# Kernel tuning notes

Hardware: AMD Instinct MI355X
Metric: run time of the kernel (lower is better)

Reference implementation:

```python
import jax, jax.numpy as jnp
from jax import lax
import numpy as np

B, V, S, K = 16, 8, 256, 66  # batch, predicates/example, seq len, num BIO tags


def setup_inputs() -> dict:
    key = jax.random.key(0)
    ks = jax.random.split(key, 9)
    return {
        "log_pa": jax.random.normal(ks[0], (B, S, S, K), jnp.float32),
        "score": jax.random.normal(ks[1], (B, S, S, K), jnp.float32),
        "v_label": jax.random.randint(ks[2], (B, V), 0, S, jnp.int32),
        "v_l": jnp.full((B,), V, jnp.int32),
        "orig_l": jax.random.randint(ks[3], (B,), S // 2, S + 1, jnp.int32),
        "role_label": jax.random.randint(ks[4], (B, V, S), 0, K, jnp.int32),
        "start_transitions": jax.random.normal(ks[5], (K,), jnp.float32),
        "transitions": jax.random.normal(ks[6], (K, K), jnp.float32),
        "end_transitions": jax.random.normal(ks[7], (K,), jnp.float32),
    }


def crf_log_likelihood(logits, tags, mask, start_t, trans, end_t):
    """allennlp ConditionalRandomField.forward: sum_n log p(tags_n | logits_n).
    logits [N,T,K] float, tags [N,T] int, mask [N,T] bool."""
    maskf = mask.astype(logits.dtype)

    # --- partition function via forward algorithm (sequential logsumexp scan) ---
    def alpha_step(alpha, x):
        logit_t, m_t = x  # [N,K], [N]
        # inner[n,i,j] = alpha[n,i] + trans[i,j] + logit_t[n,j]
        inner = alpha[:, :, None] + trans[None, :, :] + logit_t[:, None, :]
        new = jax.nn.logsumexp(inner, axis=1)  # [N,K]
        return jnp.where(m_t[:, None], new, alpha), None

    alpha0 = start_t[None, :] + logits[:, 0]  # [N,K]
    xs = (jnp.swapaxes(logits[:, 1:], 0, 1), jnp.swapaxes(mask[:, 1:], 0, 1))
    alpha, _ = lax.scan(alpha_step, alpha0, xs)
    log_z = jax.nn.logsumexp(alpha + end_t[None, :], axis=-1)  # [N]

    # --- joint score of gold path ---
    emit = jnp.take_along_axis(logits, tags[:, :, None].astype(jnp.int32), axis=2)[:, :, 0]  # [N,T]
    trans_sc = trans[tags[:, :-1], tags[:, 1:]]  # [N,T-1]
    score = start_t[tags[:, 0]]
    score = score + jnp.sum(emit[:, :-1] * maskf[:, :-1] + trans_sc * maskf[:, 1:], axis=1)
    last_idx = jnp.sum(mask.astype(jnp.int32), axis=1) - 1  # [N]
    last_tags = jnp.take_along_axis(tags, last_idx[:, None], axis=1)[:, 0]
    score = score + end_t[last_tags] + emit[:, -1] * maskf[:, -1]

    return jnp.sum(score - log_z)


def reference(log_pa, score, v_label, v_l, orig_l, role_label,
              start_transitions, transitions, end_transitions):
    # use_gold_predicate == 1 path of CRFLoss.forward, max_orig_l padded to S.
    # gather per-predicate score rows: a_score[b,k] = score[b, v_label[b,k]]
    a_score = score[jnp.arange(B)[:, None], v_label]          # [B,V,S,K]
    a_score = a_score.reshape(B * V, S, K)

    pos = jnp.arange(S)
    valid = pos[None, :] < orig_l[:, None]                    # [B,S] ragged length mask
    a_mask = jnp.broadcast_to(valid[:, None, :], (B, V, S)).reshape(B * V, S)
    a_gold = jnp.where(valid[:, None, :], role_label, 0).reshape(B * V, S)

    llh = crf_log_likelihood(a_score, a_gold, a_mask,
                             start_transitions, transitions, end_transitions)
    num_prop = B * V  # sum(v_l) with fixed V per example
    loss = llh / jnp.float32(num_prop)

    pred_idx = jnp.argmax(log_pa, axis=-1)  # [B,S,S] quick greedy decode
    return loss, pred_idx
```

## Files before the change

### kernel.cpp

```cpp
#include <hip/hip_runtime.h>
#include <cfloat>

#define Bdim 16
#define Vdim 8
#define Sdim 256
#define Kdim 66
#define NSEQ 128
#define TPB 256
#define NROW (Bdim * Sdim * Sdim)
#define ROWS_PER_BLK 128
#define AMAX_BLOCKS (NROW / ROWS_PER_BLK)
#define CHUNK 64
#define CHUNK_F (CHUNK * Kdim)
#define CHUNK_V4 (CHUNK_F / 4)

__device__ __forceinline__ void lds_fence_wave() {
  asm volatile("" ::: "memory");
  __builtin_amdgcn_wave_barrier();
  asm volatile("" ::: "memory");
}

__global__ __launch_bounds__(TPB) void crf_fused(
    const float* __restrict__ log_pa,
    const float* __restrict__ score,
    const int*   __restrict__ v_label,
    const int*   __restrict__ orig_l,
    const int*   __restrict__ role_label,
    const float* __restrict__ start_t,
    const float* __restrict__ trans,
    const float* __restrict__ end_t,
    float* __restrict__ out,
    float* __restrict__ ws)
{
  __shared__ __align__(16) float sBuf[2][CHUNK_F];
  __shared__ __align__(16) float sP[68];
  __shared__ float sGoldW[4];
  __shared__ int   sG[Sdim];

  const int tid = threadIdx.x;
  const int bid = blockIdx.x;

  if (bid >= NSEQ) {
    const int ab = bid - NSEQ;
    float* sA = &sBuf[0][0];
    const float4* g4 = reinterpret_cast<const float4*>(log_pa + (size_t)ab * ROWS_PER_BLK * Kdim);
    float4* s4 = reinterpret_cast<float4*>(sA);
#pragma unroll
    for (int f = tid; f < 2 * CHUNK_V4; f += TPB) s4[f] = g4[f];
    __syncthreads();
    if (tid < ROWS_PER_BLK) {
      const float2* row2 = reinterpret_cast<const float2*>(sA + tid * Kdim);
      float best = -FLT_MAX; int bi = 0;
#pragma unroll
      for (int q = 0; q < 33; ++q) {
        float2 v = row2[q];
        if (v.x > best) { best = v.x; bi = 2 * q; }
        if (v.y > best) { best = v.y; bi = 2 * q + 1; }
      }
      out[1 + (size_t)ab * ROWS_PER_BLK + tid] = (float)bi;
    }
    return;
  }

  const int n  = bid;
  const int b  = n / Vdim;
  const int v  = n % Vdim;
  const int L  = orig_l[b];
  const int sl = v_label[b * Vdim + v];
  const float* logits = score + (size_t)(b * Sdim + sl) * Sdim * Kdim;

  {
    float4* dst = reinterpret_cast<float4*>(sBuf[0]);
    const float4* src = reinterpret_cast<const float4*>(logits);
    for (int f = tid; f < CHUNK_V4; f += TPB) dst[f] = src[f];
    sG[tid] = role_label[(size_t)n * Sdim + tid];
  }
  __syncthreads();

  const int lane = tid;
  float Ecol[Kdim];
  float T64 = 0.f, T65 = 0.f, C44 = 0.f, C45 = 0.f, C54 = 0.f, C55 = 0.f;
  float alphaA = 0.f, alpha64 = 0.f, alpha65 = 0.f;

  if (tid < 64) {
#pragma unroll
    for (int i = 0; i < Kdim; ++i) Ecol[i] = __expf(trans[i * Kdim + lane]);
    T64 = __expf(trans[lane * Kdim + 64]);
    T65 = __expf(trans[lane * Kdim + 65]);
    C44 = __expf(trans[64 * Kdim + 64]); C45 = __expf(trans[64 * Kdim + 65]);
    C54 = __expf(trans[65 * Kdim + 64]); C55 = __expf(trans[65 * Kdim + 65]);
    alphaA = start_t[lane] + sBuf[0][lane];
    if (lane == 0) {
      alpha64 = start_t[64] + sBuf[0][64];
      alpha65 = start_t[65] + sBuf[0][65];
    }
  } else {
    int idx = tid - 64;
    float acc = 0.f;
    for (int t = idx; t < Sdim; t += 192) {
      if (t < L) {
        int g = sG[t];
        float e = logits[t * Kdim + g];
        if (t > 0) e += trans[sG[t - 1] * Kdim + g];
        acc += e;
      }
    }
#pragma unroll
    for (int off = 32; off > 0; off >>= 1) acc += __shfl_xor(acc, off, 64);
    if ((tid & 63) == 0) sGoldW[tid >> 6] = acc;
  }

  for (int c = 0; c < 4; ++c) {
    if (tid >= 64) {
      if (c < 3) {
        float4* dst = reinterpret_cast<float4*>(sBuf[(c + 1) & 1]);
        const float4* src = reinterpret_cast<const float4*>(logits + (size_t)(c + 1) * CHUNK_F);
        for (int f = tid - 64; f < CHUNK_V4; f += 192) dst[f] = src[f];
      }
    } else {
      const float* bufc = sBuf[c & 1];
      const int t0 = (c == 0) ? 1 : c * CHUNK;
      const int t1 = min(L, (c + 1) * CHUNK);
      const float4* sP4 = reinterpret_cast<const float4*>(sP);
      for (int t = t0; t < t1; ++t) {
        const float* rowp = bufc + (t - c * CHUNK) * Kdim;
        float lt = rowp[lane];
        float m  = __shfl(alphaA, 0, 64);
        float pA = __expf(alphaA - m);
        float p64 = 0.f, p65 = 0.f;
        sP[lane] = pA;
        if (lane == 0) {
          p64 = __expf(alpha64 - m);
          p65 = __expf(alpha65 - m);
          sP[64] = p64; sP[65] = p65;
        }
        lds_fence_wave();
        float s0 = 0.f, s1 = 0.f, s2 = 0.f, s3 = 0.f;
#pragma unroll
        for (int q = 0; q < 16; ++q) {
          float4 p = sP4[q];
          s0 = fmaf(p.x, Ecol[4 * q + 0], s0);
          s1 = fmaf(p.y, Ecol[4 * q + 1], s1);
          s2 = fmaf(p.z, Ecol[4 * q + 2], s2);
          s3 = fmaf(p.w, Ecol[4 * q + 3], s3);
        }
        s0 = fmaf(sP[64], Ecol[64], s0);
        s1 = fmaf(sP[65], Ecol[65], s1);
        float dot = (s0 + s1) + (s2 + s3);
        float s64 = pA * T64, s65 = pA * T65;
#pragma unroll
        for (int off = 32; off > 0; off >>= 1) {
          s64 += __shfl_xor(s64, off, 64);
          s65 += __shfl_xor(s65, off, 64);
        }
        alphaA = m + __logf(dot) + lt;
        if (lane == 0) {
          s64 += p64 * C44 + p65 * C54;
          s65 += p64 * C45 + p65 * C55;
          alpha64 = m + __logf(s64) + rowp[64];
          alpha65 = m + __logf(s65) + rowp[65];
        }
        lds_fence_wave();
      }
    }
    __syncthreads();
  }

  if (tid < 64) {
    sP[lane] = alphaA + end_t[lane];
    if (lane == 0) {
      sP[64] = alpha64 + end_t[64];
      sP[65] = alpha65 + end_t[65];
    }
    lds_fence_wave();
    if (lane == 0) {
      float M = -FLT_MAX;
      for (int i = 0; i < Kdim; ++i) M = fmaxf(M, sP[i]);
      float S = 0.f;
      for (int i = 0; i < Kdim; ++i) S += __expf(sP[i] - M);
      float logz = M + __logf(S);
      float gold = sGoldW[1] + sGoldW[2] + sGoldW[3]
                 + start_t[sG[0]] + end_t[sG[L - 1]];
      ws[n] = gold - logz;
    }
  }
}

__global__ void finalize_loss(const float* __restrict__ ws, float* __restrict__ out) {
  __shared__ float r[NSEQ];
  int tid = threadIdx.x;
  r[tid] = ws[tid];
  __syncthreads();
  for (int off = NSEQ / 2; off > 0; off >>= 1) {
    if (tid < off) r[tid] += r[tid + off];
    __syncthreads();
  }
  if (tid == 0) out[0] = r[0] / (float)NSEQ;
}

extern "C" void kernel_launch(void* const* d_in, const int* in_sizes, int n_in,
                              void* d_out, int out_size, void* d_ws, size_t ws_size,
                              hipStream_t stream) {
  const float* log_pa     = (const float*)d_in[0];
  const float* score      = (const float*)d_in[1];
  const int*   v_label    = (const int*)d_in[2];
  const int*   orig_l     = (const int*)d_in[4];
  const int*   role_label = (const int*)d_in[5];
  const float* start_t    = (const float*)d_in[6];
  const float* trans      = (const float*)d_in[7];
  const float* end_t      = (const float*)d_in[8];
  float* out = (float*)d_out;
  float* ws  = (float*)d_ws;

  dim3 grid(NSEQ + AMAX_BLOCKS);
  crf_fused<<<grid, TPB, 0, stream>>>(log_pa, score, v_label, orig_l, role_label,
                                      start_t, trans, end_t, out, ws);
  finalize_loss<<<1, NSEQ, 0, stream>>>(ws, out);
}
```

Baseline: 533.3 us.

## Run CRF forward recursion in scaled probability space instead of log space

Replaces the per-step log/exp forward algorithm with a scaled linear-space recursion. Normalized probabilities q are carried across steps, the next step's exp(emission) is prefetched, the step is normalized by q0 via a reciprocal, and the scale logs are accumulated. The two extra tags are spread over lanes 0 and 1 rather than all sitting on lane 0. The final logsumexp becomes a wave shuffle reduction. The argmax loop is also rewritten as a scalar loop. This takes the log and exp off the serial dependency chain, at the cost of relying on q0 never underflowing.

```diff
diff --git a/kernel.cpp b/kernel.cpp
--- a/kernel.cpp
+++ b/kernel.cpp
@@ -45,17 +45,15 @@
     float* sA = &sBuf[0][0];
     const float4* g4 = reinterpret_cast<const float4*>(log_pa + (size_t)ab * ROWS_PER_BLK * Kdim);
     float4* s4 = reinterpret_cast<float4*>(sA);
-#pragma unroll
     for (int f = tid; f < 2 * CHUNK_V4; f += TPB) s4[f] = g4[f];
     __syncthreads();
     if (tid < ROWS_PER_BLK) {
-      const float2* row2 = reinterpret_cast<const float2*>(sA + tid * Kdim);
-      float best = -FLT_MAX; int bi = 0;
-#pragma unroll
-      for (int q = 0; q < 33; ++q) {
-        float2 v = row2[q];
-        if (v.x > best) { best = v.x; bi = 2 * q; }
-        if (v.y > best) { best = v.y; bi = 2 * q + 1; }
+      const float* row = sA + tid * Kdim;
+      float best = row[0]; int bi = 0;
+#pragma unroll
+      for (int e = 1; e < Kdim; ++e) {
+        float vv = row[e];
+        if (vv > best) { best = vv; bi = e; }
       }
       out[1 + (size_t)ab * ROWS_PER_BLK + tid] = (float)bi;
     }
@@ -79,21 +77,22 @@
 
   const int lane = tid;
   float Ecol[Kdim];
-  float T64 = 0.f, T65 = 0.f, C44 = 0.f, C45 = 0.f, C54 = 0.f, C55 = 0.f;
-  float alphaA = 0.f, alpha64 = 0.f, alpha65 = 0.f;
+  float T64 = 0.f, T65 = 0.f, CA = 0.f, CB = 0.f;
+  float q = 0.f, qEx = 0.f, logscale = 0.f;
 
   if (tid < 64) {
 #pragma unroll
     for (int i = 0; i < Kdim; ++i) Ecol[i] = __expf(trans[i * Kdim + lane]);
     T64 = __expf(trans[lane * Kdim + 64]);
     T65 = __expf(trans[lane * Kdim + 65]);
-    C44 = __expf(trans[64 * Kdim + 64]); C45 = __expf(trans[64 * Kdim + 65]);
-    C54 = __expf(trans[65 * Kdim + 64]); C55 = __expf(trans[65 * Kdim + 65]);
-    alphaA = start_t[lane] + sBuf[0][lane];
-    if (lane == 0) {
-      alpha64 = start_t[64] + sBuf[0][64];
-      alpha65 = start_t[65] + sBuf[0][65];
-    }
+    int ex = 64 + (lane & 1);
+    CA = __expf(trans[ex * Kdim + 64]);
+    CB = __expf(trans[ex * Kdim + 65]);
+    float a0 = start_t[lane] + sBuf[0][lane];
+    float m0 = __shfl(a0, 0, 64);
+    q = __expf(a0 - m0);
+    if (lane < 2) qEx = __expf(start_t[64 + lane] + sBuf[0][64 + lane] - m0);
+    logscale = m0;
   } else {
     int idx = tid - 64;
     float acc = 0.f;
@@ -119,66 +118,65 @@
       }
     } else {
       const float* bufc = sBuf[c & 1];
-      const int t0 = (c == 0) ? 1 : c * CHUNK;
-      const int t1 = min(L, (c + 1) * CHUNK);
-      const float4* sP4 = reinterpret_cast<const float4*>(sP);
-      for (int t = t0; t < t1; ++t) {
-        const float* rowp = bufc + (t - c * CHUNK) * Kdim;
-        float lt = rowp[lane];
-        float m  = __shfl(alphaA, 0, 64);
-        float pA = __expf(alphaA - m);
-        float p64 = 0.f, p65 = 0.f;
-        sP[lane] = pA;
-        if (lane == 0) {
-          p64 = __expf(alpha64 - m);
-          p65 = __expf(alpha65 - m);
-          sP[64] = p64; sP[65] = p65;
+      const int base = c * CHUNK;
+      const int t0 = (c == 0) ? 1 : base;
+      const int t1 = min(L, base + CHUNK);
+      if (t0 < t1) {
+        const float4* sP4 = reinterpret_cast<const float4*>(sP);
+        float d   = __expf(bufc[(t0 - base) * Kdim + lane]);
+        float dEx = (lane < 2) ? __expf(bufc[(t0 - base) * Kdim + 64 + lane]) : 0.f;
+        for (int t = t0; t < t1; ++t) {
+          sP[lane] = q;
+          if (lane < 2) sP[64 + lane] = qEx;
+          lds_fence_wave();
+          float a64 = q * T64, a65 = q * T65;
+          if (lane < 2) { a64 = fmaf(qEx, CA, a64); a65 = fmaf(qEx, CB, a65); }
+          float dn = 0.f, dExn = 0.f;
+          if (t + 1 < t1) {
+            dn = __expf(bufc[(t + 1 - base) * Kdim + lane]);
+            if (lane < 2) dExn = __expf(bufc[(t + 1 - base) * Kdim + 64 + lane]);
+          }
+#pragma unroll
+          for (int off = 32; off > 0; off >>= 1) {
+            a64 += __shfl_xor(a64, off, 64);
+            a65 += __shfl_xor(a65, off, 64);
+          }
+          float4 p0 = sP4[0];
+          float q0  = p0.x;
+          float inv = __builtin_amdgcn_rcpf(q0);
+          float s0 = p0.x * Ecol[0];
+          float s1 = p0.y * Ecol[1];
+          float s2 = p0.z * Ecol[2];
+          float s3 = p0.w * Ecol[3];
+#pragma unroll
+          for (int qq = 1; qq < 16; ++qq) {
+            float4 p = sP4[qq];
+            s0 = fmaf(p.x, Ecol[4 * qq + 0], s0);
+            s1 = fmaf(p.y, Ecol[4 * qq + 1], s1);
+            s2 = fmaf(p.z, Ecol[4 * qq + 2], s2);
+            s3 = fmaf(p.w, Ecol[4 * qq + 3], s3);
+          }
+          s0 = fmaf(sP[64], Ecol[64], s0);
+          s1 = fmaf(sP[65], Ecol[65], s1);
+          float dot = (s0 + s1) + (s2 + s3);
+          logscale += __logf(q0);
+          q = dot * inv * d;
+          if (lane < 2) qEx = ((lane == 0) ? a64 : a65) * inv * dEx;
+          d = dn; dEx = dExn;
+          lds_fence_wave();
         }
-        lds_fence_wave();
-        float s0 = 0.f, s1 = 0.f, s2 = 0.f, s3 = 0.f;
-#pragma unroll
-        for (int q = 0; q < 16; ++q) {
-          float4 p = sP4[q];
-          s0 = fmaf(p.x, Ecol[4 * q + 0], s0);
-          s1 = fmaf(p.y, Ecol[4 * q + 1], s1);
-          s2 = fmaf(p.z, Ecol[4 * q + 2], s2);
-          s3 = fmaf(p.w, Ecol[4 * q + 3], s3);
-        }
-        s0 = fmaf(sP[64], Ecol[64], s0);
-        s1 = fmaf(sP[65], Ecol[65], s1);
-        float dot = (s0 + s1) + (s2 + s3);
-        float s64 = pA * T64, s65 = pA * T65;
-#pragma unroll
-        for (int off = 32; off > 0; off >>= 1) {
-          s64 += __shfl_xor(s64, off, 64);
-          s65 += __shfl_xor(s65, off, 64);
-        }
-        alphaA = m + __logf(dot) + lt;
-        if (lane == 0) {
-          s64 += p64 * C44 + p65 * C54;
-          s65 += p64 * C45 + p65 * C55;
-          alpha64 = m + __logf(s64) + rowp[64];
-          alpha65 = m + __logf(s65) + rowp[65];
-        }
-        lds_fence_wave();
       }
     }
     __syncthreads();
   }
 
   if (tid < 64) {
-    sP[lane] = alphaA + end_t[lane];
+    float z = q * __expf(end_t[lane]);
+    if (lane < 2) z = fmaf(qEx, __expf(end_t[64 + lane]), z);
+#pragma unroll
+    for (int off = 32; off > 0; off >>= 1) z += __shfl_xor(z, off, 64);
     if (lane == 0) {
-      sP[64] = alpha64 + end_t[64];
-      sP[65] = alpha65 + end_t[65];
-    }
-    lds_fence_wave();
-    if (lane == 0) {
-      float M = -FLT_MAX;
-      for (int i = 0; i < Kdim; ++i) M = fmaxf(M, sP[i]);
-      float S = 0.f;
-      for (int i = 0; i < Kdim; ++i) S += __expf(sP[i] - M);
-      float logz = M + __logf(S);
+      float logz = logscale + __logf(z);
       float gold = sGoldW[1] + sGoldW[2] + sGoldW[3]
                  + start_t[sG[0]] + end_t[sG[L - 1]];
       ws[n] = gold - logz;
```

New measurement: 574.2 us. +7.7%, slower.
